# Kernel tuning notes

Measured on AMD Instinct MI355X. Metric: run time of the kernel, lower is better.

Reference implementation:

```python
import jax, jax.numpy as jnp
import numpy as np

# dims
BS, N, B, C, D_COL, D_PCM, EXP = 4, 512, 8, 8, 128, 32, 4
G = B * C              # 64 cortical columns
D_HID = D_COL * EXP    # 512
SURPRISE_SCALE = 1.0
EPS_LN = 1e-5
EPS_NORM = 1e-6


def _unit_normalize(x):
    return x / (jnp.linalg.norm(x, axis=-1, keepdims=True) + EPS_NORM)


def _glin(x, W, b):
    # grouped linear: x [BS,N,G,Din], W [G,Din,Dout], b [G,Dout]
    return jnp.einsum('bngi,gio->bngo', x, W) + b


def setup_inputs() -> dict:
    key = jax.random.key(0)
    ks = jax.random.split(key, 12)
    s = 0.02
    return {
        'x_col': jax.random.normal(ks[0], (BS, N, G, D_COL), jnp.float32),
        'z_hat_prev': jax.random.normal(ks[1], (BS, N, G, D_PCM), jnp.float32),
        'gamma': jnp.ones((G, D_COL), jnp.float32),
        'beta': jnp.zeros((G, D_COL), jnp.float32),
        'W_up': jax.random.normal(ks[2], (G, D_COL, D_HID), jnp.float32) * s,
        'b_up': jnp.zeros((G, D_HID), jnp.float32),
        'W_down': jax.random.normal(ks[3], (G, D_HID, D_COL), jnp.float32) * s,
        'b_down': jnp.zeros((G, D_COL), jnp.float32),
        'W_post': jax.random.normal(ks[4], (G, D_COL, 4 * D_COL + 1), jnp.float32) * s,
        'b_post': jnp.zeros((G, 4 * D_COL + 1), jnp.float32),
        'W_enc': jax.random.normal(ks[5], (G, D_COL, D_PCM), jnp.float32) * s,
        'b_enc': jnp.zeros((G, D_PCM), jnp.float32),
        'W_pred': jax.random.normal(ks[6], (G, D_PCM, D_PCM), jnp.float32) * s,
        'b_pred': jnp.zeros((G, D_PCM), jnp.float32),
        'W_gain': jnp.zeros((G, D_PCM, D_COL), jnp.float32),  # nn.init.zeros_
        'b_gain': jnp.zeros((G, D_COL), jnp.float32),
    }


def reference(x_col, z_hat_prev, gamma, beta, W_up, b_up, W_down, b_down,
              W_post, b_post, W_enc, b_enc, W_pred, b_pred, W_gain, b_gain):
    # --- PCM: encode, cross-pass surprise, gain ---
    z = _glin(x_col, W_enc, b_enc)                      # [BS,N,G,D_pcm]
    delta = z - z_hat_prev
    surprise = jnp.linalg.norm(delta, axis=-1)          # [BS,N,G]
    gain = 1.0 + 0.1 * jnp.tanh(_glin(delta, W_gain, b_gain))  # [BS,N,G,D_col]

    # --- grouped LayerNorm over D_col with per-group affine ---
    mu = jnp.mean(x_col, axis=-1, keepdims=True)
    var = jnp.mean(jnp.square(x_col - mu), axis=-1, keepdims=True)
    h = (x_col - mu) * jax.lax.rsqrt(var + EPS_LN) * gamma + beta
    h = h * gain

    # --- grouped FFN with residual ---
    h = _glin(jax.nn.gelu(_glin(h, W_up, b_up), approximate=False), W_down, b_down)
    x_out = x_col + h                                   # [BS,N,G,D_col]

    # --- PCM prediction for next pass ---
    z_hat = _glin(z, W_pred, b_pred)                    # [BS,N,G,D_pcm]

    # --- fused post projection + split ---
    proj = _glin(x_out, W_post, b_post)                 # [BS,N,G,4*D_col+1]
    proj5 = proj.reshape(BS, N, B, C, 4 * D_COL + 1)
    k_pre = proj5[..., :D_COL]
    v_post = proj5[..., D_COL:2 * D_COL]
    k_cand_raw = proj5[..., 2 * D_COL:3 * D_COL]
    v_cand = proj5[..., 3 * D_COL:4 * D_COL]
    nov_raw = proj5[..., 4 * D_COL:]

    k_cand = _unit_normalize(k_pre)
    surprise5 = surprise.reshape(BS, N, B, C)
    gate = jnp.clip(surprise5 / SURPRISE_SCALE, 0.0, 1.0)
    q_nov = _unit_normalize(k_cand_raw)
    w_nov = jax.nn.sigmoid(nov_raw[..., 0])

    return (x_out, z, z_hat, surprise, k_cand, v_post, gate, q_nov, v_cand, w_nov, surprise5)
```

## Files before the change

kernel.cpp:

```cpp
#include <hip/hip_runtime.h>

typedef unsigned short u16;
typedef __attribute__((ext_vector_type(4))) unsigned short u16x4;
typedef __attribute__((ext_vector_type(8))) short short8;
typedef __attribute__((ext_vector_type(16))) float f32x16;

#define MFMA(a,b,c) __builtin_amdgcn_mfma_f32_32x32x16_bf16((a),(b),(c),0,0,0)

static constexpr size_t OFF_XOUT = 0;
static constexpr size_t OFF_Z    = 16777216;
static constexpr size_t OFF_ZHAT = 20971520;
static constexpr size_t OFF_SUR  = 25165824;
static constexpr size_t OFF_KC   = 25296896;
static constexpr size_t OFF_VP   = 42074112;
static constexpr size_t OFF_GATE = 58851328;
static constexpr size_t OFF_QN   = 58982400;
static constexpr size_t OFF_VC   = 75759616;
static constexpr size_t OFF_WN   = 92536832;
static constexpr size_t OFF_S5   = 92667904;

static constexpr size_t WUP_I = 0;
static constexpr size_t WDN_I = 4194304;
static constexpr size_t WPO_I = 8388608;
static constexpr size_t WEN_I = 12591104;
static constexpr size_t WGN_I = 12853248;
static constexpr size_t WPR_I = 13115392;

__device__ __forceinline__ u16 f2b(float f) {
    unsigned u = __float_as_uint(f);
    unsigned r = (u + 0x7FFFu + ((u >> 16) & 1u)) >> 16;
    return (u16)r;
}
__device__ __forceinline__ float b2f(u16 b) {
    return __uint_as_float(((unsigned)b) << 16);
}
__device__ __forceinline__ int swz256(int row, int b) {
    return row * 256 + (b ^ ((row & 7) << 4) ^ (((row >> 3) & 1) << 7));
}
__device__ __forceinline__ int swz64(int row, int b) {
    return row * 64 + (b ^ ((row & 3) << 4));
}
__device__ __forceinline__ short8 fragLd256(const u16* s, int row, int ks) {
    int b = ks * 32 + ((threadIdx.x >> 5) & 1) * 16;
    return *(const short8*)((const char*)s + swz256(row, b));
}
__device__ __forceinline__ short8 fragLd64(const u16* s, int row, int ks) {
    int b = ks * 32 + ((threadIdx.x >> 5) & 1) * 16;
    return *(const short8*)((const char*)s + swz64(row, b));
}
__device__ __forceinline__ float tanh_f(float x) {
    float xc = fminf(fmaxf(x, -15.f), 15.f);
    float e = __expf(2.f * xc);
    return __fdividef(e - 1.f, e + 1.f);
}
__device__ __forceinline__ float gelu_f(float u) {
    return __fdividef(u, 1.f + __expf(-1.702f * u));
}

__device__ __forceinline__ size_t mapElem(int wt, int k, int c) {
    switch (wt) {
    case 0: return (size_t)(c >> 7) * 16384 + (swz256(c & 127, 2 * k) >> 1);
    case 1: return (size_t)(k >> 7) * 16384 + (swz256(c, 2 * (k & 127)) >> 1);
    case 2: return (c == 512) ? (size_t)65536 + k
                              : (size_t)(c >> 7) * 16384 + (swz256(c & 127, 2 * k) >> 1);
    case 3: return (size_t)(swz256(c, 2 * k) >> 1);
    case 4: return (size_t)(swz64(c, 2 * k) >> 1);
    default: return (size_t)(swz64(c, 2 * k) >> 1);
    }
}

__global__ __launch_bounds__(256)
void kconv_all(const float* __restrict__ W_up, const float* __restrict__ W_down,
               const float* __restrict__ W_post, const float* __restrict__ W_enc,
               const float* __restrict__ W_gain, const float* __restrict__ W_pred,
               u16* __restrict__ ws)
{
    int b = blockIdx.x;
    const float* src; u16* dst; int K, C, bx, wt; size_t gstride;
    if (b < 1024)      { src = W_up;   dst = ws + WUP_I; K = 128; C = 512; bx = 8; wt = 0; gstride = 65536; }
    else if (b < 2048) { b -= 1024; src = W_down; dst = ws + WDN_I; K = 512; C = 128; bx = 2; wt = 1; gstride = 65536; }
    else if (b < 3200) { b -= 2048; src = W_post; dst = ws + WPO_I; K = 128; C = 513; bx = 9; wt = 2; gstride = 65664; }
    else if (b < 3328) { b -= 3200; src = W_enc;  dst = ws + WEN_I; K = 128; C = 32;  bx = 1; wt = 3; gstride = 4096; }
    else if (b < 3456) { b -= 3328; src = W_gain; dst = ws + WGN_I; K = 32;  C = 128; bx = 2; wt = 4; gstride = 4096; }
    else               { b -= 3456; src = W_pred; dst = ws + WPR_I; K = 32;  C = 32;  bx = 1; wt = 5; gstride = 1024; }
    const int by = (K + 63) >> 6;
    const int nb = bx * by;
    const int g = b / nb, r = b % nb;
    const int c0 = (r % bx) * 64, k0 = (r / bx) * 64;

    __shared__ float sT[64][65];
    const float* s = src + (size_t)g * K * C;
    u16* d = dst + (size_t)g * gstride;
    for (int e = threadIdx.x; e < 64 * 64; e += 256) {
        int kk = e >> 6, cc = e & 63;
        if (k0 + kk < K && c0 + cc < C)
            sT[kk][cc] = s[(size_t)(k0 + kk) * C + c0 + cc];
    }
    __syncthreads();
    for (int e = threadIdx.x; e < 512; e += 256) {
        int cc = e & 63, kb = e >> 6;
        int c = c0 + cc, k = k0 + kb * 8;
        if (c < C && c != 512 && k + 7 < K) {
            short8 v;
            #pragma unroll
            for (int i = 0; i < 8; ++i) v[i] = (short)f2b(sT[kb * 8 + i][cc]);
            *(short8*)(d + mapElem(wt, k, c)) = v;
        }
    }
    if (wt == 2 && c0 == 512) {
        for (int kk = threadIdx.x; kk < 64; kk += 256) {
            int k = k0 + kk;
            if (k < K) d[(size_t)65536 + k] = f2b(sT[kk][0]);
        }
    }
}

__global__ __launch_bounds__(1024, 4)
void kfused(const float* __restrict__ x_col,
            const float* __restrict__ z_hat_prev,
            const float* __restrict__ gamma,
            const float* __restrict__ beta,
            const float* __restrict__ b_enc,
            const float* __restrict__ b_pred,
            const float* __restrict__ b_gain,
            const float* __restrict__ b_up,
            const float* __restrict__ b_down,
            const float* __restrict__ b_post,
            const u16* __restrict__ ws,
            float* __restrict__ out)
{
    const int bid = blockIdx.x;
    const int xc = bid & 7, j = bid >> 3;
    const int g = xc * 8 + (j >> 4);
    const int tile = j & 15;
    const int m0 = tile * 128;

    const int tid = threadIdx.x, lane = tid & 63;
    const int w16 = tid >> 6;
    const int wr = w16 >> 2;
    const int wc = w16 & 3;
    const int l31 = lane & 31, lh = lane >> 5;

    __shared__ u16 sX[16384];
    __shared__ u16 sH[16384];
    __shared__ u16 sW[16384];
    __shared__ u16 sU[16384];
    __shared__ float sMu[128], sRstd[128], sNrm[128], sNov[128];

    u16* sWe = sW;
    u16* sWg = sW + 8192;
    u16* sWp = sW + 12288;
    u16* sD  = sU;
    u16* sZ  = sU + 4096;

    const u16* wUp = ws + WUP_I + (size_t)g * 65536;
    const u16* wDn = ws + WDN_I + (size_t)g * 65536;
    const u16* wPo = ws + WPO_I + (size_t)g * 65664;

    for (int idx = tid; idx < 128 * 32; idx += 1024) {
        int row = idx >> 5, q = idx & 31;
        float4 v = *(const float4*)&x_col[(size_t)(m0 + row) * 8192 + g * 128 + q * 4];
        u16x4 bv; bv.x = f2b(v.x); bv.y = f2b(v.y); bv.z = f2b(v.z); bv.w = f2b(v.w);
        *(u16x4*)((char*)sX + swz256(row, q * 8)) = bv;
    }
    {
        const short8* se = (const short8*)(ws + WEN_I + (size_t)g * 4096);
        const short8* sg = (const short8*)(ws + WGN_I + (size_t)g * 4096);
        const short8* sp = (const short8*)(ws + WPR_I + (size_t)g * 1024);
        if (tid < 512) ((short8*)sWe)[tid] = se[tid];
        else           ((short8*)sWg)[tid - 512] = sg[tid - 512];
        if (tid < 128) ((short8*)sWp)[tid] = sp[tid];
    }
    if (tid < 128) sNov[tid] = b2f(wPo[65536 + tid]);

    short8 pfA, pfB;
    {
        const short8* su = (const short8*)wUp;
        pfA = su[tid]; pfB = su[tid + 1024];
    }
    __syncthreads();

    if (w16 < 4) {
        f32x16 zacc = (f32x16)0.f;
        #pragma unroll
        for (int ks = 0; ks < 8; ++ks)
            zacc = MFMA(fragLd256(sX, 32 * w16 + l31, ks), fragLd256(sWe, l31, ks), zacc);
        float benc = b_enc[g * 32 + l31];
        #pragma unroll
        for (int r = 0; r < 16; ++r) {
            float zv = zacc[r] + benc;
            int row = 32 * w16 + (r & 3) + 8 * (r >> 2) + 4 * lh;
            size_t zoff = (size_t)(m0 + row) * 2048 + g * 32 + l31;
            out[OFF_Z + zoff] = zv;
            float d = zv - z_hat_prev[zoff];
            *(u16*)((char*)sD + swz64(row, l31 * 2)) = f2b(d);
            *(u16*)((char*)sZ + swz64(row, l31 * 2)) = f2b(zv);
            float ss = d * d;
            ss += __shfl_xor(ss, 1); ss += __shfl_xor(ss, 2); ss += __shfl_xor(ss, 4);
            ss += __shfl_xor(ss, 8); ss += __shfl_xor(ss, 16);
            if (l31 == 0) {
                float sur = sqrtf(ss);
                size_t p = (size_t)(m0 + row) * 64 + g;
                out[OFF_SUR + p] = sur;
                out[OFF_S5 + p] = sur;
                out[OFF_GATE + p] = fminf(fmaxf(sur, 0.f), 1.f);
            }
        }
    } else if (w16 < 8) {
        int t = tid - 256;
        int row = t >> 1, half = t & 1;
        float s1 = 0.f, s2 = 0.f;
        #pragma unroll
        for (int i = 0; i < 8; ++i) {
            short8 v = *(const short8*)((const char*)sX + swz256(row, (half * 64 + i * 8) * 2));
            #pragma unroll
            for (int jj = 0; jj < 8; ++jj) { float x = b2f((u16)v[jj]); s1 += x; s2 += x * x; }
        }
        s1 += __shfl_xor(s1, 1); s2 += __shfl_xor(s2, 1);
        if (half == 0) {
            float mu = s1 * (1.f / 128.f);
            float var = s2 * (1.f / 128.f) - mu * mu;
            sMu[row] = mu; sRstd[row] = rsqrtf(var + 1e-5f);
        }
    }
    __syncthreads();

    if (w16 < 8) {
        const int wrg = w16 >> 1;
        const int cp  = w16 & 1;
        f32x16 gacc[2];
        gacc[0] = (f32x16)0.f; gacc[1] = (f32x16)0.f;
        #pragma unroll
        for (int ks = 0; ks < 2; ++ks) {
            short8 a = fragLd64(sD, 32 * wrg + l31, ks);
            #pragma unroll
            for (int k = 0; k < 2; ++k) {
                short8 b = fragLd64(sWg, 32 * (2 * cp + k) + l31, ks);
                gacc[k] = MFMA(a, b, gacc[k]);
            }
        }
        #pragma unroll
        for (int k = 0; k < 2; ++k) {
            int col = 32 * (2 * cp + k) + l31;
            float bg = b_gain[g * 128 + col];
            float gam = gamma[g * 128 + col];
            float bet = beta[g * 128 + col];
            #pragma unroll
            for (int r = 0; r < 16; ++r) {
                int row = 32 * wrg + (r & 3) + 8 * (r >> 2) + 4 * lh;
                float gain = 1.f + 0.1f * tanh_f(gacc[k][r] + bg);
                float xv = b2f(*(const u16*)((const char*)sX + swz256(row, col * 2)));
                float h = ((xv - sMu[row]) * sRstd[row] * gam + bet) * gain;
                *(u16*)((char*)sH + swz256(row, col * 2)) = f2b(h);
            }
        }
    } else if (w16 < 12) {
        int wp = w16 - 8;
        f32x16 pacc = (f32x16)0.f;
        #pragma unroll
        for (int ks = 0; ks < 2; ++ks) {
            short8 a = fragLd64(sZ, 32 * wp + l31, ks);
            short8 b = fragLd64(sWp, l31, ks);
            pacc = MFMA(a, b, pacc);
        }
        float bpred = b_pred[g * 32 + l31];
        #pragma unroll
        for (int r = 0; r < 16; ++r) {
            int row = 32 * wp + (r & 3) + 8 * (r >> 2) + 4 * lh;
            out[OFF_ZHAT + (size_t)(m0 + row) * 2048 + g * 32 + l31] = pacc[r] + bpred;
        }
    }

    f32x16 dacc = (f32x16)0.f;

    for (int ch = 0; ch < 4; ++ch) {
        __syncthreads();
        ((short8*)sW)[tid]        = pfA;
        ((short8*)sW)[tid + 1024] = pfB;
        {
            const short8* nxt = (const short8*)(wDn + ch * 16384);
            pfA = nxt[tid]; pfB = nxt[tid + 1024];
        }
        __syncthreads();

        f32x16 uacc = (f32x16)0.f;
        #pragma unroll
        for (int ks = 0; ks < 8; ++ks)
            uacc = MFMA(fragLd256(sH, 32 * wr + l31, ks),
                        fragLd256(sW, 32 * wc + l31, ks), uacc);
        {
            float bup = b_up[(size_t)g * 512 + ch * 128 + 32 * wc + l31];
            int colB = (32 * wc + l31) * 2;
            #pragma unroll
            for (int r = 0; r < 16; ++r) {
                int row = 32 * wr + (r & 3) + 8 * (r >> 2) + 4 * lh;
                *(u16*)((char*)sU + swz256(row, colB)) = f2b(gelu_f(uacc[r] + bup));
            }
        }
        __syncthreads();
        ((short8*)sW)[tid]        = pfA;
        ((short8*)sW)[tid + 1024] = pfB;
        {
            const short8* nxt = (const short8*)((ch < 3) ? (wUp + (ch + 1) * 16384) : wPo);
            pfA = nxt[tid]; pfB = nxt[tid + 1024];
        }
        __syncthreads();
        #pragma unroll
        for (int ks = 0; ks < 8; ++ks)
            dacc = MFMA(fragLd256(sU, 32 * wr + l31, ks),
                        fragLd256(sW, 32 * wc + l31, ks), dacc);
    }

    {
        int jc = 32 * wc + l31;
        float bd = b_down[g * 128 + jc];
        #pragma unroll
        for (int r = 0; r < 16; ++r) {
            int row = 32 * wr + (r & 3) + 8 * (r >> 2) + 4 * lh;
            size_t base = (size_t)(m0 + row) * 8192 + g * 128 + jc;
            float xo = b2f(*(const u16*)((const char*)sX + swz256(row, jc * 2)))
                       + bd + dacc[r];
            out[OFF_XOUT + base] = xo;
            *(u16*)((char*)sH + swz256(row, jc * 2)) = f2b(xo);
        }
    }

    for (int s = 0; s < 4; ++s) {
        __syncthreads();
        ((short8*)sW)[tid]        = pfA;
        ((short8*)sW)[tid + 1024] = pfB;
        if (s < 3) {
            const short8* nxt = (const short8*)(wPo + (s + 1) * 16384);
            pfA = nxt[tid]; pfB = nxt[tid + 1024];
        }
        __syncthreads();

        f32x16 acc = (f32x16)0.f;
        #pragma unroll
        for (int ks = 0; ks < 8; ++ks)
            acc = MFMA(fragLd256(sH, 32 * wr + l31, ks),
                       fragLd256(sW, 32 * wc + l31, ks), acc);
        {
            float bp = b_post[g * 513 + s * 128 + 32 * wc + l31];
            int colB = (32 * wc + l31) * 2;
            #pragma unroll
            for (int r = 0; r < 16; ++r) {
                int row = 32 * wr + (r & 3) + 8 * (r >> 2) + 4 * lh;
                *(u16*)((char*)sU + swz256(row, colB)) = f2b(acc[r] + bp);
            }
        }
        __syncthreads();

        const bool nrm = (s == 0 || s == 2);
        if (nrm) {
            int row = tid >> 3, part = tid & 7;
            float ss = 0.f;
            #pragma unroll
            for (int i = 0; i < 2; ++i) {
                short8 v = *(const short8*)((const char*)sU + swz256(row, (part * 16 + i * 8) * 2));
                #pragma unroll
                for (int jj = 0; jj < 8; ++jj) { float x = b2f((u16)v[jj]); ss += x * x; }
            }
            ss += __shfl_xor(ss, 1); ss += __shfl_xor(ss, 2); ss += __shfl_xor(ss, 4);
            if (part == 0) sNrm[row] = sqrtf(ss);
            __syncthreads();
        }
        size_t off = (s == 0) ? OFF_KC : (s == 1) ? OFF_VP : (s == 2) ? OFF_QN : OFF_VC;
        for (int idx = tid; idx < 128 * 16; idx += 1024) {
            int row = idx >> 4, slot = idx & 15;
            float inv = nrm ? __fdividef(1.f, sNrm[row] + 1e-6f) : 1.f;
            short8 v = *(const short8*)((const char*)sU + swz256(row, slot * 16));
            float4 o0, o1;
            o0.x = b2f((u16)v[0]) * inv; o0.y = b2f((u16)v[1]) * inv;
            o0.z = b2f((u16)v[2]) * inv; o0.w = b2f((u16)v[3]) * inv;
            o1.x = b2f((u16)v[4]) * inv; o1.y = b2f((u16)v[5]) * inv;
            o1.z = b2f((u16)v[6]) * inv; o1.w = b2f((u16)v[7]) * inv;
            size_t base = off + (size_t)(m0 + row) * 8192 + g * 128 + slot * 8;
            *(float4*)&out[base] = o0;
            *(float4*)&out[base + 4] = o1;
        }
    }
    __syncthreads();

    {
        int row = tid >> 3, part = tid & 7;
        float accn = 0.f;
        #pragma unroll
        for (int i = 0; i < 2; ++i) {
            short8 v = *(const short8*)((const char*)sH + swz256(row, (part * 16 + i * 8) * 2));
            #pragma unroll
            for (int jj = 0; jj < 8; ++jj) accn += b2f((u16)v[jj]) * sNov[part * 16 + i * 8 + jj];
        }
        accn += __shfl_xor(accn, 1); accn += __shfl_xor(accn, 2); accn += __shfl_xor(accn, 4);
        if (part == 0) {
            float nv = accn + b_post[g * 513 + 512];
            out[OFF_WN + (size_t)(m0 + row) * 64 + g] = __fdividef(1.f, 1.f + __expf(-nv));
        }
    }
}

extern "C" void kernel_launch(void* const* d_in, const int* in_sizes, int n_in,
                              void* d_out, int out_size, void* d_ws, size_t ws_size,
                              hipStream_t stream) {
    const float* x_col      = (const float*)d_in[0];
    const float* z_hat_prev = (const float*)d_in[1];
    const float* gamma      = (const float*)d_in[2];
    const float* beta       = (const float*)d_in[3];
    const float* W_up       = (const float*)d_in[4];
    const float* b_up       = (const float*)d_in[5];
    const float* W_down     = (const float*)d_in[6];
    const float* b_down     = (const float*)d_in[7];
    const float* W_post     = (const float*)d_in[8];
    const float* b_post     = (const float*)d_in[9];
    const float* W_enc      = (const float*)d_in[10];
    const float* b_enc      = (const float*)d_in[11];
    const float* W_pred     = (const float*)d_in[12];
    const float* b_pred     = (const float*)d_in[13];
    const float* W_gain     = (const float*)d_in[14];
    const float* b_gain     = (const float*)d_in[15];
    float* out = (float*)d_out;
    u16* ws = (u16*)d_ws;

    kconv_all<<<3520, 256, 0, stream>>>(W_up, W_down, W_post, W_enc, W_gain, W_pred, ws);
    kfused<<<1024, 1024, 0, stream>>>(x_col, z_hat_prev, gamma, beta,
                                      b_enc, b_pred, b_gain, b_up, b_down, b_post,
                                      ws, out);
}
```

Baseline: 281.2 us.

## Double-buffer weight chunks in LDS and merge X/H buffers to cut barriers

Merges the X and H shared buffers into one and keeps the residual x values in registers, which frees LDS for a second weight buffer (sW2). Weight chunks for the up, down and post projections now alternate between the two buffers, so the store of the next chunk overlaps the current MFMA work and each stage needs fewer __syncthreads. The gain GEMM is spread across all 16 waves, and the z_hat prediction moves after it. LDS use per block stays the same, but the buffer-reuse ordering becomes more delicate and any hazard would silently corrupt results.

```diff
diff --git a/kernel.cpp b/kernel.cpp
--- a/kernel.cpp
+++ b/kernel.cpp
@@ -141,17 +141,17 @@
     const int wc = w16 & 3;
     const int l31 = lane & 31, lh = lane >> 5;
 
-    __shared__ u16 sX[16384];
-    __shared__ u16 sH[16384];
+    __shared__ u16 sXH[16384];
     __shared__ u16 sW[16384];
+    __shared__ u16 sW2[16384];
     __shared__ u16 sU[16384];
     __shared__ float sMu[128], sRstd[128], sNrm[128], sNov[128];
 
     u16* sWe = sW;
     u16* sWg = sW + 8192;
-    u16* sWp = sW + 12288;
     u16* sD  = sU;
     u16* sZ  = sU + 4096;
+    u16* sWp = sU + 8192;
 
     const u16* wUp = ws + WUP_I + (size_t)g * 65536;
     const u16* wDn = ws + WDN_I + (size_t)g * 65536;
@@ -161,7 +161,7 @@
         int row = idx >> 5, q = idx & 31;
         float4 v = *(const float4*)&x_col[(size_t)(m0 + row) * 8192 + g * 128 + q * 4];
         u16x4 bv; bv.x = f2b(v.x); bv.y = f2b(v.y); bv.z = f2b(v.z); bv.w = f2b(v.w);
-        *(u16x4*)((char*)sX + swz256(row, q * 8)) = bv;
+        *(u16x4*)((char*)sXH + swz256(row, q * 8)) = bv;
     }
     {
         const short8* se = (const short8*)(ws + WEN_I + (size_t)g * 4096);
@@ -174,17 +174,14 @@
     if (tid < 128) sNov[tid] = b2f(wPo[65536 + tid]);
 
     short8 pfA, pfB;
-    {
-        const short8* su = (const short8*)wUp;
-        pfA = su[tid]; pfB = su[tid + 1024];
-    }
+    { const short8* p = (const short8*)wUp; pfA = p[tid]; pfB = p[tid + 1024]; }
     __syncthreads();
 
     if (w16 < 4) {
         f32x16 zacc = (f32x16)0.f;
         #pragma unroll
         for (int ks = 0; ks < 8; ++ks)
-            zacc = MFMA(fragLd256(sX, 32 * w16 + l31, ks), fragLd256(sWe, l31, ks), zacc);
+            zacc = MFMA(fragLd256(sXH, 32 * w16 + l31, ks), fragLd256(sWe, l31, ks), zacc);
         float benc = b_enc[g * 32 + l31];
         #pragma unroll
         for (int r = 0; r < 16; ++r) {
@@ -212,7 +209,7 @@
         float s1 = 0.f, s2 = 0.f;
         #pragma unroll
         for (int i = 0; i < 8; ++i) {
-            short8 v = *(const short8*)((const char*)sX + swz256(row, (half * 64 + i * 8) * 2));
+            short8 v = *(const short8*)((const char*)sXH + swz256(row, (half * 64 + i * 8) * 2));
             #pragma unroll
             for (int jj = 0; jj < 8; ++jj) { float x = b2f((u16)v[jj]); s1 += x; s2 += x * x; }
         }
@@ -225,69 +222,60 @@
     }
     __syncthreads();
 
-    if (w16 < 8) {
-        const int wrg = w16 >> 1;
-        const int cp  = w16 & 1;
-        f32x16 gacc[2];
-        gacc[0] = (f32x16)0.f; gacc[1] = (f32x16)0.f;
-        #pragma unroll
-        for (int ks = 0; ks < 2; ++ks) {
-            short8 a = fragLd64(sD, 32 * wrg + l31, ks);
-            #pragma unroll
-            for (int k = 0; k < 2; ++k) {
-                short8 b = fragLd64(sWg, 32 * (2 * cp + k) + l31, ks);
-                gacc[k] = MFMA(a, b, gacc[k]);
-            }
-        }
-        #pragma unroll
-        for (int k = 0; k < 2; ++k) {
-            int col = 32 * (2 * cp + k) + l31;
-            float bg = b_gain[g * 128 + col];
-            float gam = gamma[g * 128 + col];
-            float bet = beta[g * 128 + col];
-            #pragma unroll
-            for (int r = 0; r < 16; ++r) {
-                int row = 32 * wrg + (r & 3) + 8 * (r >> 2) + 4 * lh;
-                float gain = 1.f + 0.1f * tanh_f(gacc[k][r] + bg);
-                float xv = b2f(*(const u16*)((const char*)sX + swz256(row, col * 2)));
-                float h = ((xv - sMu[row]) * sRstd[row] * gam + bet) * gain;
-                *(u16*)((char*)sH + swz256(row, col * 2)) = f2b(h);
-            }
-        }
-    } else if (w16 < 12) {
-        int wp = w16 - 8;
+    float xres[16];
+    {
+        f32x16 gacc = (f32x16)0.f;
+        #pragma unroll
+        for (int ks = 0; ks < 2; ++ks)
+            gacc = MFMA(fragLd64(sD, 32 * wr + l31, ks),
+                        fragLd64(sWg, 32 * wc + l31, ks), gacc);
+        int col = 32 * wc + l31;
+        float bg = b_gain[g * 128 + col];
+        float gam = gamma[g * 128 + col];
+        float bet = beta[g * 128 + col];
+        #pragma unroll
+        for (int r = 0; r < 16; ++r) {
+            int row = 32 * wr + (r & 3) + 8 * (r >> 2) + 4 * lh;
+            float xv = b2f(*(const u16*)((const char*)sXH + swz256(row, col * 2)));
+            xres[r] = xv;
+            float gain = 1.f + 0.1f * tanh_f(gacc[r] + bg);
+            float h = ((xv - sMu[row]) * sRstd[row] * gam + bet) * gain;
+            *(u16*)((char*)sXH + swz256(row, col * 2)) = f2b(h);
+        }
+    }
+    __syncthreads();
+
+    ((short8*)sW)[tid]        = pfA;
+    ((short8*)sW)[tid + 1024] = pfB;
+    { const short8* p = (const short8*)wDn; pfA = p[tid]; pfB = p[tid + 1024]; }
+    if (w16 < 4) {
         f32x16 pacc = (f32x16)0.f;
         #pragma unroll
-        for (int ks = 0; ks < 2; ++ks) {
-            short8 a = fragLd64(sZ, 32 * wp + l31, ks);
-            short8 b = fragLd64(sWp, l31, ks);
-            pacc = MFMA(a, b, pacc);
-        }
+        for (int ks = 0; ks < 2; ++ks)
+            pacc = MFMA(fragLd64(sZ, 32 * w16 + l31, ks), fragLd64(sWp, l31, ks), pacc);
         float bpred = b_pred[g * 32 + l31];
         #pragma unroll
         for (int r = 0; r < 16; ++r) {
-            int row = 32 * wp + (r & 3) + 8 * (r >> 2) + 4 * lh;
+            int row = 32 * w16 + (r & 3) + 8 * (r >> 2) + 4 * lh;
             out[OFF_ZHAT + (size_t)(m0 + row) * 2048 + g * 32 + l31] = pacc[r] + bpred;
         }
     }
+    __syncthreads();
 
     f32x16 dacc = (f32x16)0.f;
 
     for (int ch = 0; ch < 4; ++ch) {
-        __syncthreads();
-        ((short8*)sW)[tid]        = pfA;
-        ((short8*)sW)[tid + 1024] = pfB;
+        f32x16 uacc = (f32x16)0.f;
+        #pragma unroll
+        for (int ks = 0; ks < 8; ++ks)
+            uacc = MFMA(fragLd256(sXH, 32 * wr + l31, ks),
+                        fragLd256(sW, 32 * wc + l31, ks), uacc);
+        ((short8*)sW2)[tid]        = pfA;
+        ((short8*)sW2)[tid + 1024] = pfB;
         {
-            const short8* nxt = (const short8*)(wDn + ch * 16384);
-            pfA = nxt[tid]; pfB = nxt[tid + 1024];
-        }
-        __syncthreads();
-
-        f32x16 uacc = (f32x16)0.f;
-        #pragma unroll
-        for (int ks = 0; ks < 8; ++ks)
-            uacc = MFMA(fragLd256(sH, 32 * wr + l31, ks),
-                        fragLd256(sW, 32 * wc + l31, ks), uacc);
+            const short8* p = (const short8*)((ch < 3) ? (wUp + (ch + 1) * 16384) : wPo);
+            pfA = p[tid]; pfB = p[tid + 1024];
+        }
         {
             float bup = b_up[(size_t)g * 512 + ch * 128 + 32 * wc + l31];
             int colB = (32 * wc + l31) * 2;
@@ -298,17 +286,18 @@
             }
         }
         __syncthreads();
-        ((short8*)sW)[tid]        = pfA;
-        ((short8*)sW)[tid + 1024] = pfB;
-        {
-            const short8* nxt = (const short8*)((ch < 3) ? (wUp + (ch + 1) * 16384) : wPo);
-            pfA = nxt[tid]; pfB = nxt[tid + 1024];
-        }
-        __syncthreads();
+
         #pragma unroll
         for (int ks = 0; ks < 8; ++ks)
             dacc = MFMA(fragLd256(sU, 32 * wr + l31, ks),
-                        fragLd256(sW, 32 * wc + l31, ks), dacc);
+                        fragLd256(sW2, 32 * wc + l31, ks), dacc);
+        if (ch < 3) {
+            ((short8*)sW)[tid]        = pfA;
+            ((short8*)sW)[tid + 1024] = pfB;
+            const short8* p = (const short8*)(wDn + (ch + 1) * 16384);
+            pfA = p[tid]; pfB = p[tid + 1024];
+            __syncthreads();
+        }
     }
 
     {
@@ -318,28 +307,24 @@
         for (int r = 0; r < 16; ++r) {
             int row = 32 * wr + (r & 3) + 8 * (r >> 2) + 4 * lh;
             size_t base = (size_t)(m0 + row) * 8192 + g * 128 + jc;
-            float xo = b2f(*(const u16*)((const char*)sX + swz256(row, jc * 2)))
-                       + bd + dacc[r];
+            float xo = xres[r] + bd + dacc[r];
             out[OFF_XOUT + base] = xo;
-            *(u16*)((char*)sH + swz256(row, jc * 2)) = f2b(xo);
-        }
-    }
-
-    for (int s = 0; s < 4; ++s) {
-        __syncthreads();
+            *(u16*)((char*)sXH + swz256(row, jc * 2)) = f2b(xo);
+        }
         ((short8*)sW)[tid]        = pfA;
         ((short8*)sW)[tid + 1024] = pfB;
-        if (s < 3) {
-            const short8* nxt = (const short8*)(wPo + (s + 1) * 16384);
-            pfA = nxt[tid]; pfB = nxt[tid + 1024];
-        }
-        __syncthreads();
-
+        const short8* p = (const short8*)(wPo + 16384);
+        pfA = p[tid]; pfB = p[tid + 1024];
+    }
+    __syncthreads();
+
+    for (int s = 0; s < 4; ++s) {
+        const u16* buf = (s & 1) ? sW2 : sW;
         f32x16 acc = (f32x16)0.f;
         #pragma unroll
         for (int ks = 0; ks < 8; ++ks)
-            acc = MFMA(fragLd256(sH, 32 * wr + l31, ks),
-                       fragLd256(sW, 32 * wc + l31, ks), acc);
+            acc = MFMA(fragLd256(sXH, 32 * wr + l31, ks),
+                       fragLd256(buf, 32 * wc + l31, ks), acc);
         {
             float bp = b_post[g * 513 + s * 128 + 32 * wc + l31];
             int colB = (32 * wc + l31) * 2;
@@ -347,6 +332,15 @@
             for (int r = 0; r < 16; ++r) {
                 int row = 32 * wr + (r & 3) + 8 * (r >> 2) + 4 * lh;
                 *(u16*)((char*)sU + swz256(row, colB)) = f2b(acc[r] + bp);
+            }
+        }
+        if (s < 3) {
+            u16* other = (s & 1) ? sW : sW2;
+            ((short8*)other)[tid]        = pfA;
+            ((short8*)other)[tid + 1024] = pfB;
+            if (s < 2) {
+                const short8* p = (const short8*)(wPo + (s + 2) * 16384);
+                pfA = p[tid]; pfB = p[tid + 1024];
             }
         }
         __syncthreads();
@@ -379,15 +373,15 @@
             *(float4*)&out[base] = o0;
             *(float4*)&out[base + 4] = o1;
         }
-    }
-    __syncthreads();
+        if (s < 3) __syncthreads();
+    }
 
     {
         int row = tid >> 3, part = tid & 7;
         float accn = 0.f;
         #pragma unroll
         for (int i = 0; i < 2; ++i) {
-            short8 v = *(const short8*)((const char*)sH + swz256(row, (part * 16 + i * 8) * 2));
+            short8 v = *(const short8*)((const char*)sXH + swz256(row, (part * 16 + i * 8) * 2));
             #pragma unroll
             for (int jj = 0; jj < 8; ++jj) accn += b2f((u16)v[jj]) * sNov[part * 16 + i * 8 + jj];
         }
```

Measured after the change: 338.5 us. 20.4% more time.
